# Performance work log

Hardware: AMD Instinct MI355X
Metric: run time of the kernel (lower is better)

The kernel has to match this reference:

```python
import jax, jax.numpy as jnp
import numpy as np

B, N, E = 4, 10000, 160000
NODE_DIM, EDGE_DIM, HIDDEN, HEADS = 128, 64, 256, 8
HEAD_DIM = HIDDEN // HEADS
LN_EPS = 1e-5


def setup_inputs() -> dict:
    key = jax.random.key(0)
    ks = jax.random.split(key, 11)
    s = 0.05  # stand-in for xavier scale
    return {
        "node_feat": jax.random.normal(ks[0], (B, N, NODE_DIM), dtype=jnp.float32),
        "edge_index": jax.random.randint(ks[1], (2, E), 0, N, dtype=jnp.int64),
        "edge_attr": jax.random.normal(ks[2], (B, E, EDGE_DIM), dtype=jnp.float32),
        "W_node": jax.random.normal(ks[3], (NODE_DIM, HIDDEN), dtype=jnp.float32) * s,
        "W_edge": jax.random.normal(ks[4], (EDGE_DIM, HIDDEN), dtype=jnp.float32) * s,
        "W_res": jax.random.normal(ks[5], (NODE_DIM, HIDDEN), dtype=jnp.float32) * s,
        "att_src": jax.random.normal(ks[6], (HEADS, HEAD_DIM), dtype=jnp.float32) * s,
        "att_dst": jax.random.normal(ks[7], (HEADS, HEAD_DIM), dtype=jnp.float32) * s,
        "att_edge": jax.random.normal(ks[8], (HEADS, HEAD_DIM), dtype=jnp.float32) * s,
        "ln_gamma": jnp.ones((HIDDEN,), dtype=jnp.float32),
        "ln_beta": jnp.zeros((HIDDEN,), dtype=jnp.float32),
    }


def reference(node_feat, edge_index, edge_attr, W_node, W_edge, W_res,
              att_src, att_dst, att_edge, ln_gamma, ln_beta):
    b, n, _ = node_feat.shape
    e_cnt = edge_attr.shape[1]
    src = edge_index[0]
    dst = edge_index[1]

    h = (node_feat @ W_node).reshape(b, n, HEADS, HEAD_DIM)          # [B,N,H,D]
    e = (edge_attr @ W_edge).reshape(b, e_cnt, HEADS, HEAD_DIM)       # [B,E,H,D]
    h_src = h[:, src]                                                 # [B,E,H,D]
    h_dst = h[:, dst]                                                 # [B,E,H,D]

    logits = (jnp.einsum('behd,hd->beh', h_src, att_src)
              + jnp.einsum('behd,hd->beh', h_dst, att_dst)
              + jnp.einsum('behd,hd->beh', e, att_edge))              # [B,E,H]
    logits = jax.nn.leaky_relu(logits, negative_slope=0.2)

    # segment softmax over edges grouped by dst node (edge-leading layout)
    lt = logits.transpose(1, 0, 2)                                    # [E,B,H]
    seg_max = jax.ops.segment_max(lt, dst, num_segments=n)            # [N,B,H]
    ex = jnp.exp(lt - seg_max[dst])
    seg_sum = jax.ops.segment_sum(ex, dst, num_segments=n)            # [N,B,H]
    alpha = ex / seg_sum[dst]                                         # [E,B,H]

    msg = alpha[..., None] * (h_src + e).transpose(1, 0, 2, 3)        # [E,B,H,D]
    agg = jax.ops.segment_sum(msg, dst, num_segments=n)               # [N,B,H,D]
    out = agg.transpose(1, 0, 2, 3).reshape(b, n, HIDDEN)             # [B,N,HIDDEN]

    x = out + node_feat @ W_res
    mu = jnp.mean(x, axis=-1, keepdims=True)
    var = jnp.mean(jnp.square(x - mu), axis=-1, keepdims=True)
    x = (x - mu) * jax.lax.rsqrt(var + LN_EPS) * ln_gamma + ln_beta
    return jax.nn.elu(x)
```

## Files before the change

### kernel.cpp

```cpp
#include <hip/hip_runtime.h>

#define BB 4
#define NN 10000
#define EE 160000
#define HID 256
#define NHEAD 8

typedef __attribute__((ext_vector_type(8))) short short8v;
typedef __attribute__((ext_vector_type(4))) float f32x4;

__device__ __forceinline__ unsigned short f2bf(float f) {
  unsigned u = __float_as_uint(f);
  unsigned r = (u + 0x7fffu + ((u >> 16) & 1u)) >> 16;
  return (unsigned short)r;
}
__device__ __forceinline__ float bf2f(unsigned short u) {
  return __uint_as_float(((unsigned)u) << 16);
}

__global__ __launch_bounds__(512) void k_prep(
    const float* __restrict__ We, const float* __restrict__ ae,
    const float* __restrict__ Wn, const float* __restrict__ Wr,
    float* __restrict__ What, unsigned short* __restrict__ We16,
    unsigned short* __restrict__ Bpack) {
  const int t = threadIdx.x;
  if (blockIdx.x == 32) {
    int k = t >> 3, hh = t & 7;
    float s = 0.f;
#pragma unroll
    for (int d = 0; d < 32; ++d) s += We[k * HID + hh * 32 + d] * ae[hh * 32 + d];
    What[k * NHEAD + hh] = s;
    for (int j = t; j < 64 * HID; j += 512) We16[j] = f2bf(We[j]);
    return;
  }
  if (t >= 256) return;
  const int nt = blockIdx.x;
  const int ks = t >> 6;
  const int l = t & 63;
  const int k0 = ks * 32 + (l >> 4) * 8;
  const float* __restrict__ src = (nt < 16) ? Wn : Wr;
  const int c2 = (nt * 16 + (l & 15)) & 255;
  short8v v;
#pragma unroll
  for (int e = 0; e < 8; ++e) v[e] = f2bf(src[(k0 + e) * HID + c2]);
  *reinterpret_cast<short8v*>(Bpack + ((size_t)(nt * 4 + ks) * 64 + l) * 8) = v;
}

__global__ __launch_bounds__(512) void k_projm(
    const float* __restrict__ nf, const unsigned short* __restrict__ Bpack,
    const float* __restrict__ as_, const float* __restrict__ ad_,
    unsigned short* __restrict__ h16, float* __restrict__ out,
    float* __restrict__ ssrc, float* __restrict__ sdst) {
  const int t = threadIdx.x;
  const int w = t >> 6, l = t & 63;
  const int base = blockIdx.x * 64 + (w & 3) * 16;
  const int nhalf = w >> 2;
  const int arow = base + (l & 15);
  short8v a[4];
#pragma unroll
  for (int ks = 0; ks < 4; ++ks) {
    const float* p = nf + (size_t)arow * 128 + ks * 32 + (l >> 4) * 8;
    const float4 f0 = *reinterpret_cast<const float4*>(p);
    const float4 f1 = *reinterpret_cast<const float4*>(p + 4);
    short8v v;
    v[0] = f2bf(f0.x); v[1] = f2bf(f0.y); v[2] = f2bf(f0.z); v[3] = f2bf(f0.w);
    v[4] = f2bf(f1.x); v[5] = f2bf(f1.y); v[6] = f2bf(f1.z); v[7] = f2bf(f1.w);
    a[ks] = v;
  }
  f32x4 acc[16];
#pragma unroll
  for (int i = 0; i < 16; ++i) acc[i] = (f32x4){0.f, 0.f, 0.f, 0.f};
  const short8v* bp =
      reinterpret_cast<const short8v*>(Bpack) + (size_t)nhalf * 4096 + l;
#pragma unroll
  for (int nt = 0; nt < 16; ++nt) {
#pragma unroll
    for (int ks = 0; ks < 4; ++ks) {
      const short8v bf = bp[(nt * 4 + ks) * 64];
      acc[nt] = __builtin_amdgcn_mfma_f32_16x16x32_bf16(a[ks], bf, acc[nt], 0, 0, 0);
    }
  }
  unsigned short* __restrict__ resOv = reinterpret_cast<unsigned short*>(out);
#pragma unroll
  for (int b = 0; b < 4; ++b) {
    const int bn = base + (l >> 4) * 4 + b;
    if (nhalf == 0) {
      const int bb = bn / NN, n = bn - bb * NN;
      unsigned short* __restrict__ rowp = h16 + (((size_t)n * 4 + bb) << 8);
#pragma unroll
      for (int nt = 0; nt < 16; ++nt) rowp[nt * 16 + (l & 15)] = f2bf(acc[nt][b]);
    } else {
      unsigned short* __restrict__ rowp = resOv + ((size_t)bn << 9);
#pragma unroll
      for (int nt = 0; nt < 16; ++nt) rowp[nt * 16 + (l & 15)] = f2bf(acc[nt][b]);
    }
  }
  if (nhalf == 0) {
    const int lo = l & 15;
#pragma unroll
    for (int h = 0; h < 8; ++h) {
      const float a0 = as_[h * 32 + lo], a1 = as_[h * 32 + 16 + lo];
      const float d0 = ad_[h * 32 + lo], d1 = ad_[h * 32 + 16 + lo];
#pragma unroll
      for (int rb = 0; rb < 4; ++rb) {
        float ps = acc[2 * h][rb] * a0 + acc[2 * h + 1][rb] * a1;
        float pd = acc[2 * h][rb] * d0 + acc[2 * h + 1][rb] * d1;
#pragma unroll
        for (int off = 1; off <= 8; off <<= 1) {
          ps += __shfl_xor(ps, off);
          pd += __shfl_xor(pd, off);
        }
        if (lo == 0) {
          const int bn = base + (l >> 4) * 4 + rb;
          ssrc[(size_t)bn * NHEAD + h] = ps;
          sdst[(size_t)bn * NHEAD + h] = pd;
        }
      }
    }
  }
}

__global__ void k_hist(const int* __restrict__ ei, int* __restrict__ cnt) {
  int e = blockIdx.x * 256 + threadIdx.x;
  if (e < EE) atomicAdd(&cnt[ei[EE + e]], 1);
}

__global__ __launch_bounds__(1024) void k_scan(const int* __restrict__ cnt,
                                               int* __restrict__ off) {
  __shared__ int ls[1024];
  const int t = threadIdx.x;
  int own = 0;
  int deg[10];
  if (t < 1000) {
#pragma unroll
    for (int i = 0; i < 10; ++i) { deg[i] = cnt[t * 10 + i]; own += deg[i]; }
  }
  ls[t] = own;
  __syncthreads();
  for (int s = 1; s < 1024; s <<= 1) {
    int v = 0;
    if (t >= s) v = ls[t - s];
    __syncthreads();
    if (t >= s) ls[t] += v;
    __syncthreads();
  }
  if (t < 1000) {
    int start = ls[t] - own;
#pragma unroll
    for (int i = 0; i < 10; ++i) { off[t * 10 + i] = start; start += deg[i]; }
  }
  if (t == 0) off[NN] = EE;
}

__global__ void k_scatter(const int* __restrict__ ei, const int* __restrict__ off,
                          int* __restrict__ cur, int2* __restrict__ eidx,
                          int* __restrict__ inv) {
  int e = blockIdx.x * 256 + threadIdx.x;
  if (e >= EE) return;
  int s = ei[e], d = ei[EE + e];
  int pos = off[d] + atomicAdd(&cur[d], 1);
  eidx[pos] = make_int2(e, s);
  inv[e] = pos;
}

__global__ __launch_bounds__(256) void k_elogit(
    const float* __restrict__ ea, const int* __restrict__ ei,
    const float* __restrict__ What, const float* __restrict__ ssrc,
    const float* __restrict__ sdst, const int* __restrict__ inv,
    float* __restrict__ exP) {
  __shared__ float sea[32 * 65];
  __shared__ float sw[64 * NHEAD];
  const int t = threadIdx.x;
  sw[t] = What[t];
  sw[t + 256] = What[t + 256];
  const int g0 = blockIdx.x * 32;
  const float* base = ea + (size_t)g0 * 64;
#pragma unroll
  for (int j = 0; j < 8; ++j) {
    int f = t + j * 256;
    sea[(f >> 6) * 65 + (f & 63)] = base[f];
  }
  __syncthreads();
  const int il = t >> 3, hh = t & 7;
  const int g = g0 + il;
  float acc = 0.f;
#pragma unroll
  for (int k = 0; k < 64; ++k) acc += sea[il * 65 + k] * sw[k * NHEAD + hh];
  const int b = g / EE, e = g - b * EE;
  const int src = ei[e], dst = ei[EE + e];
  float lg = ssrc[((size_t)b * NN + src) * NHEAD + hh] +
             sdst[((size_t)b * NN + dst) * NHEAD + hh] + acc;
  lg = lg > 0.f ? lg : 0.2f * lg;
  const int pos = inv[e];
  exP[(((size_t)pos * 4 + b) << 3) + hh] = __expf(lg);
}

__global__ __launch_bounds__(256) void k_agg(
    const float* __restrict__ ea, const unsigned short* __restrict__ h16,
    const float* __restrict__ exP, const int* __restrict__ off,
    const int2* __restrict__ eidx, const unsigned short* __restrict__ We16,
    const float* __restrict__ gam, const float* __restrict__ bet,
    float* __restrict__ out) {
  __shared__ float zsh[4][8 * 65];
  const int wid = threadIdx.x >> 6, l = threadIdx.x & 63;
  const int b = wid, node = blockIdx.x;
  const int start = off[node], end = off[node + 1];
  const int hq = l >> 3;
  const int hr = l & 7;
  float4 u4 = {0.f, 0.f, 0.f, 0.f};
  float z0 = 0.f, z1 = 0.f, z2 = 0.f, z3 = 0.f;
  float z4 = 0.f, z5 = 0.f, z6 = 0.f, z7 = 0.f;
  float ss = 0.f;
  const float* __restrict__ exb = exP + ((size_t)b << 3);
  const float* __restrict__ eab = ea + (size_t)b * EE * 64;
  const unsigned short* __restrict__ hb = h16 + ((size_t)b << 8);
#pragma unroll 8
  for (int i = start; i < end; ++i) {
    const int2 es = eidx[i];
    const float* exi = exb + ((size_t)i << 5);
    const float4 xa = *reinterpret_cast<const float4*>(exi);
    const float4 xb = *reinterpret_cast<const float4*>(exi + 4);
    const float exu = exi[hq];
    ss += exi[hr];
    const float eal = eab[(size_t)es.x * 64 + l];
    const ushort4 h4 =
        *reinterpret_cast<const ushort4*>(hb + ((size_t)es.y << 10) + 4 * l);
    z0 += xa.x * eal; z1 += xa.y * eal; z2 += xa.z * eal; z3 += xa.w * eal;
    z4 += xb.x * eal; z5 += xb.y * eal; z6 += xb.z * eal; z7 += xb.w * eal;
    u4.x += exu * bf2f(h4.x); u4.y += exu * bf2f(h4.y);
    u4.z += exu * bf2f(h4.z); u4.w += exu * bf2f(h4.w);
  }
  zsh[wid][0 * 65 + l] = z0; zsh[wid][1 * 65 + l] = z1;
  zsh[wid][2 * 65 + l] = z2; zsh[wid][3 * 65 + l] = z3;
  zsh[wid][4 * 65 + l] = z4; zsh[wid][5 * 65 + l] = z5;
  zsh[wid][6 * 65 + l] = z6; zsh[wid][7 * 65 + l] = z7;
  const size_t bn = (size_t)b * NN + node;
  const ushort4 r16 = *reinterpret_cast<const ushort4*>(
      reinterpret_cast<const unsigned short*>(out) + (bn << 9) + 4 * l);
#pragma unroll 8
  for (int k = 0; k < 64; ++k) {
    const float zk = zsh[wid][hq * 65 + k];
    const ushort4 wv = *reinterpret_cast<const ushort4*>(We16 + (k << 8) + 4 * l);
    u4.x += zk * bf2f(wv.x); u4.y += zk * bf2f(wv.y);
    u4.z += zk * bf2f(wv.z); u4.w += zk * bf2f(wv.w);
  }
  const float ssq = __shfl(ss, hq);
  const float sc = ssq > 0.f ? 1.f / ssq : 0.f;
  u4.x = u4.x * sc + bf2f(r16.x); u4.y = u4.y * sc + bf2f(r16.y);
  u4.z = u4.z * sc + bf2f(r16.z); u4.w = u4.w * sc + bf2f(r16.w);
  float s1 = u4.x + u4.y + u4.z + u4.w;
  float s2 = u4.x * u4.x + u4.y * u4.y + u4.z * u4.z + u4.w * u4.w;
#pragma unroll
  for (int off2 = 1; off2 <= 32; off2 <<= 1) {
    s1 += __shfl_xor(s1, off2);
    s2 += __shfl_xor(s2, off2);
  }
  const float mu = s1 * (1.f / HID);
  const float var = s2 * (1.f / HID) - mu * mu;
  const float rstd = rsqrtf(var + 1e-5f);
  const float4 g4 = reinterpret_cast<const float4*>(gam)[l];
  const float4 b4 = reinterpret_cast<const float4*>(bet)[l];
  float4 y;
  y.x = (u4.x - mu) * rstd * g4.x + b4.x;
  y.y = (u4.y - mu) * rstd * g4.y + b4.y;
  y.z = (u4.z - mu) * rstd * g4.z + b4.z;
  y.w = (u4.w - mu) * rstd * g4.w + b4.w;
  y.x = y.x > 0.f ? y.x : expm1f(y.x);
  y.y = y.y > 0.f ? y.y : expm1f(y.y);
  y.z = y.z > 0.f ? y.z : expm1f(y.z);
  y.w = y.w > 0.f ? y.w : expm1f(y.w);
  *reinterpret_cast<float4*>(out + (bn << 8) + 4 * l) = y;
}

extern "C" void kernel_launch(void* const* d_in, const int* in_sizes, int n_in,
                              void* d_out, int out_size, void* d_ws, size_t ws_size,
                              hipStream_t stream) {
  const float* nf   = (const float*)d_in[0];
  const int*   ei   = (const int*)d_in[1];
  const float* eatt = (const float*)d_in[2];
  const float* Wn   = (const float*)d_in[3];
  const float* We   = (const float*)d_in[4];
  const float* Wr   = (const float*)d_in[5];
  const float* as_  = (const float*)d_in[6];
  const float* ad_  = (const float*)d_in[7];
  const float* ae_  = (const float*)d_in[8];
  const float* gam  = (const float*)d_in[9];
  const float* bet  = (const float*)d_in[10];
  float* out = (float*)d_out;

  char* ws = (char*)d_ws;
  size_t o = 0;
  auto alloc = [&](size_t bytes) -> void* {
    void* p = ws + o;
    o += (bytes + 255) & ~(size_t)255;
    return p;
  };
  unsigned short* h16  = (unsigned short*)alloc((size_t)BB * NN * HID * 2);
  float* ssrc   = (float*)alloc((size_t)BB * NN * NHEAD * 4);
  float* sdst   = (float*)alloc((size_t)BB * NN * NHEAD * 4);
  float* What   = (float*)alloc(64 * NHEAD * 4);
  unsigned short* We16 = (unsigned short*)alloc(64 * HID * 2);
  float* exP    = (float*)alloc((size_t)BB * EE * NHEAD * 4);
  size_t cnt_off = o;
  int*  cnt     = (int*)alloc(NN * 4);
  int*  cur     = (int*)alloc(NN * 4);
  size_t cnt_bytes = o - cnt_off;
  int*  offn    = (int*)alloc((NN + 1) * 4);
  int2* eidx    = (int2*)alloc((size_t)EE * 8);
  int*  inv     = (int*)alloc((size_t)EE * 4);
  unsigned short* Bpack = (unsigned short*)alloc((size_t)512 * 128 * 2);

  hipLaunchKernelGGL(k_prep, dim3(33), dim3(512), 0, stream,
                     We, ae_, Wn, Wr, What, We16, Bpack);
  hipLaunchKernelGGL(k_projm, dim3(BB * NN / 64), dim3(512), 0, stream,
                     nf, Bpack, as_, ad_, h16, out, ssrc, sdst);
  hipMemsetAsync(ws + cnt_off, 0, cnt_bytes, stream);
  hipLaunchKernelGGL(k_hist, dim3((EE + 255) / 256), dim3(256), 0, stream, ei, cnt);
  hipLaunchKernelGGL(k_scan, dim3(1), dim3(1024), 0, stream, cnt, offn);
  hipLaunchKernelGGL(k_scatter, dim3((EE + 255) / 256), dim3(256), 0, stream,
                     ei, offn, cur, eidx, inv);
  hipLaunchKernelGGL(k_elogit, dim3(BB * EE / 32), dim3(256), 0, stream,
                     eatt, ei, What, ssrc, sdst, inv, exP);
  hipLaunchKernelGGL(k_agg, dim3(NN), dim3(256), 0, stream,
                     eatt, h16, exP, offn, eidx, We16, gam, bet, out);
}
```

Before: 282.9 us.

## Fold memset and histogram into prep/projection kernels; aggregate two nodes per block

The memset of the count and cursor arrays moves into extra blocks of the prep kernel, and the degree histogram moves into extra blocks of the projection kernel. This removes one memset and one kernel launch. The aggregation kernel now handles two destination nodes per block and interleaves their edge loops, so more independent gathers are in flight and each We16 load is reused for both nodes. The cost is higher register pressure and fewer blocks in the aggregation kernel.

```diff
diff --git a/kernel.cpp b/kernel.cpp
--- a/kernel.cpp
+++ b/kernel.cpp
@@ -22,8 +22,16 @@
     const float* __restrict__ We, const float* __restrict__ ae,
     const float* __restrict__ Wn, const float* __restrict__ Wr,
     float* __restrict__ What, unsigned short* __restrict__ We16,
-    unsigned short* __restrict__ Bpack) {
+    unsigned short* __restrict__ Bpack, int* __restrict__ cnt,
+    int* __restrict__ cur) {
   const int t = threadIdx.x;
+  if (blockIdx.x >= 33) {
+    const int zb = blockIdx.x - 33;
+    int* __restrict__ dst = (zb < 20) ? cnt : cur;
+    const int idx = (zb % 20) * 512 + t;
+    if (idx < NN) dst[idx] = 0;
+    return;
+  }
   if (blockIdx.x == 32) {
     int k = t >> 3, hh = t & 7;
     float s = 0.f;
@@ -50,8 +58,14 @@
     const float* __restrict__ nf, const unsigned short* __restrict__ Bpack,
     const float* __restrict__ as_, const float* __restrict__ ad_,
     unsigned short* __restrict__ h16, float* __restrict__ out,
-    float* __restrict__ ssrc, float* __restrict__ sdst) {
+    float* __restrict__ ssrc, float* __restrict__ sdst,
+    const int* __restrict__ ei, int* __restrict__ cnt) {
   const int t = threadIdx.x;
+  if (blockIdx.x >= 625) {
+    const int e = (blockIdx.x - 625) * 512 + t;
+    if (e < EE) atomicAdd(&cnt[ei[EE + e]], 1);
+    return;
+  }
   const int w = t >> 6, l = t & 63;
   const int base = blockIdx.x * 64 + (w & 3) * 16;
   const int nhalf = w >> 2;
@@ -118,11 +132,6 @@
       }
     }
   }
-}
-
-__global__ void k_hist(const int* __restrict__ ei, int* __restrict__ cnt) {
-  int e = blockIdx.x * 256 + threadIdx.x;
-  if (e < EE) atomicAdd(&cnt[ei[EE + e]], 1);
 }
 
 __global__ __launch_bounds__(1024) void k_scan(const int* __restrict__ cnt,
@@ -195,81 +204,125 @@
   exP[(((size_t)pos * 4 + b) << 3) + hh] = __expf(lg);
 }
 
+#define AGG_BODY(i, u4, z0, z1, z2, z3, z4, z5, z6, z7, ss)                    \
+  {                                                                            \
+    const int2 es = eidx[i];                                                   \
+    const float* exi = exb + ((size_t)(i) << 5);                               \
+    const float4 xa = *reinterpret_cast<const float4*>(exi);                   \
+    const float4 xb = *reinterpret_cast<const float4*>(exi + 4);               \
+    const float exu = exi[hq];                                                 \
+    ss += exi[hr];                                                             \
+    const float eal = eab[(size_t)es.x * 64 + l];                              \
+    const ushort4 h4 =                                                         \
+        *reinterpret_cast<const ushort4*>(hb + ((size_t)es.y << 10) + 4 * l);  \
+    z0 += xa.x * eal; z1 += xa.y * eal; z2 += xa.z * eal; z3 += xa.w * eal;    \
+    z4 += xb.x * eal; z5 += xb.y * eal; z6 += xb.z * eal; z7 += xb.w * eal;    \
+    u4.x += exu * bf2f(h4.x); u4.y += exu * bf2f(h4.y);                        \
+    u4.z += exu * bf2f(h4.z); u4.w += exu * bf2f(h4.w);                        \
+  }
+
 __global__ __launch_bounds__(256) void k_agg(
     const float* __restrict__ ea, const unsigned short* __restrict__ h16,
     const float* __restrict__ exP, const int* __restrict__ off,
     const int2* __restrict__ eidx, const unsigned short* __restrict__ We16,
     const float* __restrict__ gam, const float* __restrict__ bet,
     float* __restrict__ out) {
-  __shared__ float zsh[4][8 * 65];
+  __shared__ float zshA[4][8 * 65];
+  __shared__ float zshB[4][8 * 65];
   const int wid = threadIdx.x >> 6, l = threadIdx.x & 63;
-  const int b = wid, node = blockIdx.x;
-  const int start = off[node], end = off[node + 1];
+  const int b = wid;
+  const int nodeA = blockIdx.x * 2, nodeB = nodeA + 1;
+  const int sA = off[nodeA], eAe = off[nodeA + 1], eBe = off[nodeB + 1];
+  const int sB = eAe;
   const int hq = l >> 3;
   const int hr = l & 7;
-  float4 u4 = {0.f, 0.f, 0.f, 0.f};
-  float z0 = 0.f, z1 = 0.f, z2 = 0.f, z3 = 0.f;
-  float z4 = 0.f, z5 = 0.f, z6 = 0.f, z7 = 0.f;
-  float ss = 0.f;
+  float4 uA = {0.f, 0.f, 0.f, 0.f}, uB = {0.f, 0.f, 0.f, 0.f};
+  float zA0 = 0.f, zA1 = 0.f, zA2 = 0.f, zA3 = 0.f;
+  float zA4 = 0.f, zA5 = 0.f, zA6 = 0.f, zA7 = 0.f;
+  float zB0 = 0.f, zB1 = 0.f, zB2 = 0.f, zB3 = 0.f;
+  float zB4 = 0.f, zB5 = 0.f, zB6 = 0.f, zB7 = 0.f;
+  float ssA = 0.f, ssB = 0.f;
   const float* __restrict__ exb = exP + ((size_t)b << 3);
   const float* __restrict__ eab = ea + (size_t)b * EE * 64;
   const unsigned short* __restrict__ hb = h16 + ((size_t)b << 8);
-#pragma unroll 8
-  for (int i = start; i < end; ++i) {
-    const int2 es = eidx[i];
-    const float* exi = exb + ((size_t)i << 5);
-    const float4 xa = *reinterpret_cast<const float4*>(exi);
-    const float4 xb = *reinterpret_cast<const float4*>(exi + 4);
-    const float exu = exi[hq];
-    ss += exi[hr];
-    const float eal = eab[(size_t)es.x * 64 + l];
-    const ushort4 h4 =
-        *reinterpret_cast<const ushort4*>(hb + ((size_t)es.y << 10) + 4 * l);
-    z0 += xa.x * eal; z1 += xa.y * eal; z2 += xa.z * eal; z3 += xa.w * eal;
-    z4 += xb.x * eal; z5 += xb.y * eal; z6 += xb.z * eal; z7 += xb.w * eal;
-    u4.x += exu * bf2f(h4.x); u4.y += exu * bf2f(h4.y);
-    u4.z += exu * bf2f(h4.z); u4.w += exu * bf2f(h4.w);
-  }
-  zsh[wid][0 * 65 + l] = z0; zsh[wid][1 * 65 + l] = z1;
-  zsh[wid][2 * 65 + l] = z2; zsh[wid][3 * 65 + l] = z3;
-  zsh[wid][4 * 65 + l] = z4; zsh[wid][5 * 65 + l] = z5;
-  zsh[wid][6 * 65 + l] = z6; zsh[wid][7 * 65 + l] = z7;
-  const size_t bn = (size_t)b * NN + node;
-  const ushort4 r16 = *reinterpret_cast<const ushort4*>(
-      reinterpret_cast<const unsigned short*>(out) + (bn << 9) + 4 * l);
+  const int nA = eAe - sA, nB = eBe - sB;
+  const int nmin = nA < nB ? nA : nB;
+  for (int j = 0; j < nmin; ++j) {
+    AGG_BODY(sA + j, uA, zA0, zA1, zA2, zA3, zA4, zA5, zA6, zA7, ssA);
+    AGG_BODY(sB + j, uB, zB0, zB1, zB2, zB3, zB4, zB5, zB6, zB7, ssB);
+  }
+  for (int j = nmin; j < nA; ++j)
+    AGG_BODY(sA + j, uA, zA0, zA1, zA2, zA3, zA4, zA5, zA6, zA7, ssA);
+  for (int j = nmin; j < nB; ++j)
+    AGG_BODY(sB + j, uB, zB0, zB1, zB2, zB3, zB4, zB5, zB6, zB7, ssB);
+  zshA[wid][0 * 65 + l] = zA0; zshA[wid][1 * 65 + l] = zA1;
+  zshA[wid][2 * 65 + l] = zA2; zshA[wid][3 * 65 + l] = zA3;
+  zshA[wid][4 * 65 + l] = zA4; zshA[wid][5 * 65 + l] = zA5;
+  zshA[wid][6 * 65 + l] = zA6; zshA[wid][7 * 65 + l] = zA7;
+  zshB[wid][0 * 65 + l] = zB0; zshB[wid][1 * 65 + l] = zB1;
+  zshB[wid][2 * 65 + l] = zB2; zshB[wid][3 * 65 + l] = zB3;
+  zshB[wid][4 * 65 + l] = zB4; zshB[wid][5 * 65 + l] = zB5;
+  zshB[wid][6 * 65 + l] = zB6; zshB[wid][7 * 65 + l] = zB7;
+  const size_t bnA = (size_t)b * NN + nodeA;
+  const size_t bnB = bnA + 1;
+  const unsigned short* __restrict__ ov =
+      reinterpret_cast<const unsigned short*>(out);
+  const ushort4 rA = *reinterpret_cast<const ushort4*>(ov + (bnA << 9) + 4 * l);
+  const ushort4 rB = *reinterpret_cast<const ushort4*>(ov + (bnB << 9) + 4 * l);
 #pragma unroll 8
   for (int k = 0; k < 64; ++k) {
-    const float zk = zsh[wid][hq * 65 + k];
+    const float zkA = zshA[wid][hq * 65 + k];
+    const float zkB = zshB[wid][hq * 65 + k];
     const ushort4 wv = *reinterpret_cast<const ushort4*>(We16 + (k << 8) + 4 * l);
-    u4.x += zk * bf2f(wv.x); u4.y += zk * bf2f(wv.y);
-    u4.z += zk * bf2f(wv.z); u4.w += zk * bf2f(wv.w);
-  }
-  const float ssq = __shfl(ss, hq);
-  const float sc = ssq > 0.f ? 1.f / ssq : 0.f;
-  u4.x = u4.x * sc + bf2f(r16.x); u4.y = u4.y * sc + bf2f(r16.y);
-  u4.z = u4.z * sc + bf2f(r16.z); u4.w = u4.w * sc + bf2f(r16.w);
-  float s1 = u4.x + u4.y + u4.z + u4.w;
-  float s2 = u4.x * u4.x + u4.y * u4.y + u4.z * u4.z + u4.w * u4.w;
+    const float w0 = bf2f(wv.x), w1 = bf2f(wv.y), w2 = bf2f(wv.z), w3 = bf2f(wv.w);
+    uA.x += zkA * w0; uA.y += zkA * w1; uA.z += zkA * w2; uA.w += zkA * w3;
+    uB.x += zkB * w0; uB.y += zkB * w1; uB.z += zkB * w2; uB.w += zkB * w3;
+  }
+  const float sqA = __shfl(ssA, hq), sqB = __shfl(ssB, hq);
+  const float scA = sqA > 0.f ? 1.f / sqA : 0.f;
+  const float scB = sqB > 0.f ? 1.f / sqB : 0.f;
+  uA.x = uA.x * scA + bf2f(rA.x); uA.y = uA.y * scA + bf2f(rA.y);
+  uA.z = uA.z * scA + bf2f(rA.z); uA.w = uA.w * scA + bf2f(rA.w);
+  uB.x = uB.x * scB + bf2f(rB.x); uB.y = uB.y * scB + bf2f(rB.y);
+  uB.z = uB.z * scB + bf2f(rB.z); uB.w = uB.w * scB + bf2f(rB.w);
+  float s1A = uA.x + uA.y + uA.z + uA.w;
+  float s2A = uA.x * uA.x + uA.y * uA.y + uA.z * uA.z + uA.w * uA.w;
+  float s1B = uB.x + uB.y + uB.z + uB.w;
+  float s2B = uB.x * uB.x + uB.y * uB.y + uB.z * uB.z + uB.w * uB.w;
 #pragma unroll
   for (int off2 = 1; off2 <= 32; off2 <<= 1) {
-    s1 += __shfl_xor(s1, off2);
-    s2 += __shfl_xor(s2, off2);
-  }
-  const float mu = s1 * (1.f / HID);
-  const float var = s2 * (1.f / HID) - mu * mu;
-  const float rstd = rsqrtf(var + 1e-5f);
+    s1A += __shfl_xor(s1A, off2);
+    s2A += __shfl_xor(s2A, off2);
+    s1B += __shfl_xor(s1B, off2);
+    s2B += __shfl_xor(s2B, off2);
+  }
+  const float muA = s1A * (1.f / HID);
+  const float varA = s2A * (1.f / HID) - muA * muA;
+  const float rsA = rsqrtf(varA + 1e-5f);
+  const float muB = s1B * (1.f / HID);
+  const float varB = s2B * (1.f / HID) - muB * muB;
+  const float rsB = rsqrtf(varB + 1e-5f);
   const float4 g4 = reinterpret_cast<const float4*>(gam)[l];
   const float4 b4 = reinterpret_cast<const float4*>(bet)[l];
-  float4 y;
-  y.x = (u4.x - mu) * rstd * g4.x + b4.x;
-  y.y = (u4.y - mu) * rstd * g4.y + b4.y;
-  y.z = (u4.z - mu) * rstd * g4.z + b4.z;
-  y.w = (u4.w - mu) * rstd * g4.w + b4.w;
-  y.x = y.x > 0.f ? y.x : expm1f(y.x);
-  y.y = y.y > 0.f ? y.y : expm1f(y.y);
-  y.z = y.z > 0.f ? y.z : expm1f(y.z);
-  y.w = y.w > 0.f ? y.w : expm1f(y.w);
-  *reinterpret_cast<float4*>(out + (bn << 8) + 4 * l) = y;
+  float4 yA, yB;
+  yA.x = (uA.x - muA) * rsA * g4.x + b4.x;
+  yA.y = (uA.y - muA) * rsA * g4.y + b4.y;
+  yA.z = (uA.z - muA) * rsA * g4.z + b4.z;
+  yA.w = (uA.w - muA) * rsA * g4.w + b4.w;
+  yB.x = (uB.x - muB) * rsB * g4.x + b4.x;
+  yB.y = (uB.y - muB) * rsB * g4.y + b4.y;
+  yB.z = (uB.z - muB) * rsB * g4.z + b4.z;
+  yB.w = (uB.w - muB) * rsB * g4.w + b4.w;
+  yA.x = yA.x > 0.f ? yA.x : expm1f(yA.x);
+  yA.y = yA.y > 0.f ? yA.y : expm1f(yA.y);
+  yA.z = yA.z > 0.f ? yA.z : expm1f(yA.z);
+  yA.w = yA.w > 0.f ? yA.w : expm1f(yA.w);
+  yB.x = yB.x > 0.f ? yB.x : expm1f(yB.x);
+  yB.y = yB.y > 0.f ? yB.y : expm1f(yB.y);
+  yB.z = yB.z > 0.f ? yB.z : expm1f(yB.z);
+  yB.w = yB.w > 0.f ? yB.w : expm1f(yB.w);
+  *reinterpret_cast<float4*>(out + (bnA << 8) + 4 * l) = yA;
+  *reinterpret_cast<float4*>(out + (bnB << 8) + 4 * l) = yB;
 }
 
 extern "C" void kernel_launch(void* const* d_in, const int* in_sizes, int n_in,
@@ -301,26 +354,22 @@
   float* What   = (float*)alloc(64 * NHEAD * 4);
   unsigned short* We16 = (unsigned short*)alloc(64 * HID * 2);
   float* exP    = (float*)alloc((size_t)BB * EE * NHEAD * 4);
-  size_t cnt_off = o;
   int*  cnt     = (int*)alloc(NN * 4);
   int*  cur     = (int*)alloc(NN * 4);
-  size_t cnt_bytes = o - cnt_off;
   int*  offn    = (int*)alloc((NN + 1) * 4);
   int2* eidx    = (int2*)alloc((size_t)EE * 8);
   int*  inv     = (int*)alloc((size_t)EE * 4);
   unsigned short* Bpack = (unsigned short*)alloc((size_t)512 * 128 * 2);
 
-  hipLaunchKernelGGL(k_prep, dim3(33), dim3(512), 0, stream,
-                     We, ae_, Wn, Wr, What, We16, Bpack);
-  hipLaunchKernelGGL(k_projm, dim3(BB * NN / 64), dim3(512), 0, stream,
-                     nf, Bpack, as_, ad_, h16, out, ssrc, sdst);
-  hipMemsetAsync(ws + cnt_off, 0, cnt_bytes, stream);
-  hipLaunchKernelGGL(k_hist, dim3((EE + 255) / 256), dim3(256), 0, stream, ei, cnt);
+  hipLaunchKernelGGL(k_prep, dim3(73), dim3(512), 0, stream,
+                     We, ae_, Wn, Wr, What, We16, Bpack, cnt, cur);
+  hipLaunchKernelGGL(k_projm, dim3(625 + (EE + 511) / 512), dim3(512), 0, stream,
+                     nf, Bpack, as_, ad_, h16, out, ssrc, sdst, ei, cnt);
   hipLaunchKernelGGL(k_scan, dim3(1), dim3(1024), 0, stream, cnt, offn);
   hipLaunchKernelGGL(k_scatter, dim3((EE + 255) / 256), dim3(256), 0, stream,
                      ei, offn, cur, eidx, inv);
   hipLaunchKernelGGL(k_elogit, dim3(BB * EE / 32), dim3(256), 0, stream,
                      eatt, ei, What, ssrc, sdst, inv, exP);
-  hipLaunchKernelGGL(k_agg, dim3(NN), dim3(256), 0, stream,
+  hipLaunchKernelGGL(k_agg, dim3(NN / 2), dim3(256), 0, stream,
                      eatt, h16, exP, offn, eidx, We16, gam, bet, out);
 }
```

Measured after the change: 242.2 us, median of 2. 14.4% less time.

## Fuse counter zeroing and histogram into existing kernels; process four nodes per agg block

Applied to the files above, without the earlier changes.

Zeroing of the degree counters moves into extra blocks of the prep kernel, and the destination histogram moves into extra blocks of the projection kernel. This removes a memset and a separate kernel launch. The aggregation kernel now handles four destination nodes per block, interleaving their edge loops so more independent gathers are in flight, with the gamma/beta loads shared across nodes. The cost is much higher register pressure from four sets of accumulators, and divergence when the four nodes have different degrees.

```diff
diff --git a/kernel.cpp b/kernel.cpp
--- a/kernel.cpp
+++ b/kernel.cpp
@@ -22,8 +22,16 @@
     const float* __restrict__ We, const float* __restrict__ ae,
     const float* __restrict__ Wn, const float* __restrict__ Wr,
     float* __restrict__ What, unsigned short* __restrict__ We16,
-    unsigned short* __restrict__ Bpack) {
+    unsigned short* __restrict__ Bpack, int* __restrict__ cnt,
+    int* __restrict__ cur) {
   const int t = threadIdx.x;
+  if (blockIdx.x >= 33) {
+    const int zb = blockIdx.x - 33;
+    int* __restrict__ dst = (zb < 20) ? cnt : cur;
+    const int idx = (zb % 20) * 512 + t;
+    if (idx < NN) dst[idx] = 0;
+    return;
+  }
   if (blockIdx.x == 32) {
     int k = t >> 3, hh = t & 7;
     float s = 0.f;
@@ -50,8 +58,14 @@
     const float* __restrict__ nf, const unsigned short* __restrict__ Bpack,
     const float* __restrict__ as_, const float* __restrict__ ad_,
     unsigned short* __restrict__ h16, float* __restrict__ out,
-    float* __restrict__ ssrc, float* __restrict__ sdst) {
+    float* __restrict__ ssrc, float* __restrict__ sdst,
+    const int* __restrict__ ei, int* __restrict__ cnt) {
   const int t = threadIdx.x;
+  if (blockIdx.x >= 625) {
+    const int e = (blockIdx.x - 625) * 512 + t;
+    if (e < EE) atomicAdd(&cnt[ei[EE + e]], 1);
+    return;
+  }
   const int w = t >> 6, l = t & 63;
   const int base = blockIdx.x * 64 + (w & 3) * 16;
   const int nhalf = w >> 2;
@@ -118,11 +132,6 @@
       }
     }
   }
-}
-
-__global__ void k_hist(const int* __restrict__ ei, int* __restrict__ cnt) {
-  int e = blockIdx.x * 256 + threadIdx.x;
-  if (e < EE) atomicAdd(&cnt[ei[EE + e]], 1);
 }
 
 __global__ __launch_bounds__(1024) void k_scan(const int* __restrict__ cnt,
@@ -195,51 +204,37 @@
   exP[(((size_t)pos * 4 + b) << 3) + hh] = __expf(lg);
 }
 
-__global__ __launch_bounds__(256) void k_agg(
-    const float* __restrict__ ea, const unsigned short* __restrict__ h16,
-    const float* __restrict__ exP, const int* __restrict__ off,
-    const int2* __restrict__ eidx, const unsigned short* __restrict__ We16,
-    const float* __restrict__ gam, const float* __restrict__ bet,
-    float* __restrict__ out) {
-  __shared__ float zsh[4][8 * 65];
-  const int wid = threadIdx.x >> 6, l = threadIdx.x & 63;
-  const int b = wid, node = blockIdx.x;
-  const int start = off[node], end = off[node + 1];
-  const int hq = l >> 3;
-  const int hr = l & 7;
-  float4 u4 = {0.f, 0.f, 0.f, 0.f};
-  float z0 = 0.f, z1 = 0.f, z2 = 0.f, z3 = 0.f;
-  float z4 = 0.f, z5 = 0.f, z6 = 0.f, z7 = 0.f;
-  float ss = 0.f;
-  const float* __restrict__ exb = exP + ((size_t)b << 3);
-  const float* __restrict__ eab = ea + (size_t)b * EE * 64;
-  const unsigned short* __restrict__ hb = h16 + ((size_t)b << 8);
-#pragma unroll 8
-  for (int i = start; i < end; ++i) {
-    const int2 es = eidx[i];
-    const float* exi = exb + ((size_t)i << 5);
-    const float4 xa = *reinterpret_cast<const float4*>(exi);
-    const float4 xb = *reinterpret_cast<const float4*>(exi + 4);
-    const float exu = exi[hq];
-    ss += exi[hr];
-    const float eal = eab[(size_t)es.x * 64 + l];
-    const ushort4 h4 =
-        *reinterpret_cast<const ushort4*>(hb + ((size_t)es.y << 10) + 4 * l);
-    z0 += xa.x * eal; z1 += xa.y * eal; z2 += xa.z * eal; z3 += xa.w * eal;
-    z4 += xb.x * eal; z5 += xb.y * eal; z6 += xb.z * eal; z7 += xb.w * eal;
-    u4.x += exu * bf2f(h4.x); u4.y += exu * bf2f(h4.y);
-    u4.z += exu * bf2f(h4.z); u4.w += exu * bf2f(h4.w);
-  }
-  zsh[wid][0 * 65 + l] = z0; zsh[wid][1 * 65 + l] = z1;
-  zsh[wid][2 * 65 + l] = z2; zsh[wid][3 * 65 + l] = z3;
-  zsh[wid][4 * 65 + l] = z4; zsh[wid][5 * 65 + l] = z5;
-  zsh[wid][6 * 65 + l] = z6; zsh[wid][7 * 65 + l] = z7;
-  const size_t bn = (size_t)b * NN + node;
+#define AGG_BODY(i, u4, z0, z1, z2, z3, z4, z5, z6, z7, ss)                    \
+  {                                                                            \
+    const int2 es = eidx[i];                                                   \
+    const float* exi = exb + ((size_t)(i) << 5);                               \
+    const float4 xa = *reinterpret_cast<const float4*>(exi);                   \
+    const float4 xb = *reinterpret_cast<const float4*>(exi + 4);               \
+    const float exu = exi[hq];                                                 \
+    ss += exi[hr];                                                             \
+    const float eal = eab[(size_t)es.x * 64 + l];                              \
+    const ushort4 h4 =                                                         \
+        *reinterpret_cast<const ushort4*>(hb + ((size_t)es.y << 10) + 4 * l);  \
+    z0 += xa.x * eal; z1 += xa.y * eal; z2 += xa.z * eal; z3 += xa.w * eal;    \
+    z4 += xb.x * eal; z5 += xb.y * eal; z6 += xb.z * eal; z7 += xb.w * eal;    \
+    u4.x += exu * bf2f(h4.x); u4.y += exu * bf2f(h4.y);                        \
+    u4.z += exu * bf2f(h4.z); u4.w += exu * bf2f(h4.w);                        \
+  }
+
+__device__ __forceinline__ void agg_epilogue(
+    float* __restrict__ zrow, int l, int hq, float4 u4, float ss,
+    float z0, float z1, float z2, float z3, float z4, float z5, float z6,
+    float z7, size_t bn, const unsigned short* __restrict__ We16,
+    float4 g4, float4 b4, float* __restrict__ out) {
+  zrow[0 * 65 + l] = z0; zrow[1 * 65 + l] = z1;
+  zrow[2 * 65 + l] = z2; zrow[3 * 65 + l] = z3;
+  zrow[4 * 65 + l] = z4; zrow[5 * 65 + l] = z5;
+  zrow[6 * 65 + l] = z6; zrow[7 * 65 + l] = z7;
   const ushort4 r16 = *reinterpret_cast<const ushort4*>(
       reinterpret_cast<const unsigned short*>(out) + (bn << 9) + 4 * l);
 #pragma unroll 8
   for (int k = 0; k < 64; ++k) {
-    const float zk = zsh[wid][hq * 65 + k];
+    const float zk = zrow[hq * 65 + k];
     const ushort4 wv = *reinterpret_cast<const ushort4*>(We16 + (k << 8) + 4 * l);
     u4.x += zk * bf2f(wv.x); u4.y += zk * bf2f(wv.y);
     u4.z += zk * bf2f(wv.z); u4.w += zk * bf2f(wv.w);
@@ -258,8 +253,6 @@
   const float mu = s1 * (1.f / HID);
   const float var = s2 * (1.f / HID) - mu * mu;
   const float rstd = rsqrtf(var + 1e-5f);
-  const float4 g4 = reinterpret_cast<const float4*>(gam)[l];
-  const float4 b4 = reinterpret_cast<const float4*>(bet)[l];
   float4 y;
   y.x = (u4.x - mu) * rstd * g4.x + b4.x;
   y.y = (u4.y - mu) * rstd * g4.y + b4.y;
@@ -270,6 +263,58 @@
   y.z = y.z > 0.f ? y.z : expm1f(y.z);
   y.w = y.w > 0.f ? y.w : expm1f(y.w);
   *reinterpret_cast<float4*>(out + (bn << 8) + 4 * l) = y;
+}
+
+__global__ __launch_bounds__(256) void k_agg(
+    const float* __restrict__ ea, const unsigned short* __restrict__ h16,
+    const float* __restrict__ exP, const int* __restrict__ off,
+    const int2* __restrict__ eidx, const unsigned short* __restrict__ We16,
+    const float* __restrict__ gam, const float* __restrict__ bet,
+    float* __restrict__ out) {
+  __shared__ float zsh[4][8 * 65];
+  const int wid = threadIdx.x >> 6, l = threadIdx.x & 63;
+  const int b = wid;
+  const int node0 = blockIdx.x * 4;
+  const int s0 = off[node0], s1 = off[node0 + 1], s2 = off[node0 + 2],
+            s3 = off[node0 + 3], s4 = off[node0 + 4];
+  const int n0 = s1 - s0, n1 = s2 - s1, n2 = s3 - s2, n3 = s4 - s3;
+  int nmax = n0 > n1 ? n0 : n1;
+  nmax = nmax > n2 ? nmax : n2;
+  nmax = nmax > n3 ? nmax : n3;
+  const int hq = l >> 3;
+  const int hr = l & 7;
+  float4 uA = {0.f, 0.f, 0.f, 0.f}, uB = {0.f, 0.f, 0.f, 0.f};
+  float4 uC = {0.f, 0.f, 0.f, 0.f}, uD = {0.f, 0.f, 0.f, 0.f};
+  float zA0 = 0.f, zA1 = 0.f, zA2 = 0.f, zA3 = 0.f;
+  float zA4 = 0.f, zA5 = 0.f, zA6 = 0.f, zA7 = 0.f;
+  float zB0 = 0.f, zB1 = 0.f, zB2 = 0.f, zB3 = 0.f;
+  float zB4 = 0.f, zB5 = 0.f, zB6 = 0.f, zB7 = 0.f;
+  float zC0 = 0.f, zC1 = 0.f, zC2 = 0.f, zC3 = 0.f;
+  float zC4 = 0.f, zC5 = 0.f, zC6 = 0.f, zC7 = 0.f;
+  float zD0 = 0.f, zD1 = 0.f, zD2 = 0.f, zD3 = 0.f;
+  float zD4 = 0.f, zD5 = 0.f, zD6 = 0.f, zD7 = 0.f;
+  float ssA = 0.f, ssB = 0.f, ssC = 0.f, ssD = 0.f;
+  const float* __restrict__ exb = exP + ((size_t)b << 3);
+  const float* __restrict__ eab = ea + (size_t)b * EE * 64;
+  const unsigned short* __restrict__ hb = h16 + ((size_t)b << 8);
+  for (int j = 0; j < nmax; ++j) {
+    if (j < n0) AGG_BODY(s0 + j, uA, zA0, zA1, zA2, zA3, zA4, zA5, zA6, zA7, ssA);
+    if (j < n1) AGG_BODY(s1 + j, uB, zB0, zB1, zB2, zB3, zB4, zB5, zB6, zB7, ssB);
+    if (j < n2) AGG_BODY(s2 + j, uC, zC0, zC1, zC2, zC3, zC4, zC5, zC6, zC7, ssC);
+    if (j < n3) AGG_BODY(s3 + j, uD, zD0, zD1, zD2, zD3, zD4, zD5, zD6, zD7, ssD);
+  }
+  const float4 g4 = reinterpret_cast<const float4*>(gam)[l];
+  const float4 b4 = reinterpret_cast<const float4*>(bet)[l];
+  float* __restrict__ zrow = zsh[wid];
+  const size_t bn0 = (size_t)b * NN + node0;
+  agg_epilogue(zrow, l, hq, uA, ssA, zA0, zA1, zA2, zA3, zA4, zA5, zA6, zA7,
+               bn0 + 0, We16, g4, b4, out);
+  agg_epilogue(zrow, l, hq, uB, ssB, zB0, zB1, zB2, zB3, zB4, zB5, zB6, zB7,
+               bn0 + 1, We16, g4, b4, out);
+  agg_epilogue(zrow, l, hq, uC, ssC, zC0, zC1, zC2, zC3, zC4, zC5, zC6, zC7,
+               bn0 + 2, We16, g4, b4, out);
+  agg_epilogue(zrow, l, hq, uD, ssD, zD0, zD1, zD2, zD3, zD4, zD5, zD6, zD7,
+               bn0 + 3, We16, g4, b4, out);
 }
 
 extern "C" void kernel_launch(void* const* d_in, const int* in_sizes, int n_in,
@@ -301,26 +346,22 @@
   float* What   = (float*)alloc(64 * NHEAD * 4);
   unsigned short* We16 = (unsigned short*)alloc(64 * HID * 2);
   float* exP    = (float*)alloc((size_t)BB * EE * NHEAD * 4);
-  size_t cnt_off = o;
   int*  cnt     = (int*)alloc(NN * 4);
   int*  cur     = (int*)alloc(NN * 4);
-  size_t cnt_bytes = o - cnt_off;
   int*  offn    = (int*)alloc((NN + 1) * 4);
   int2* eidx    = (int2*)alloc((size_t)EE * 8);
   int*  inv     = (int*)alloc((size_t)EE * 4);
   unsigned short* Bpack = (unsigned short*)alloc((size_t)512 * 128 * 2);
 
-  hipLaunchKernelGGL(k_prep, dim3(33), dim3(512), 0, stream,
-                     We, ae_, Wn, Wr, What, We16, Bpack);
-  hipLaunchKernelGGL(k_projm, dim3(BB * NN / 64), dim3(512), 0, stream,
-                     nf, Bpack, as_, ad_, h16, out, ssrc, sdst);
-  hipMemsetAsync(ws + cnt_off, 0, cnt_bytes, stream);
-  hipLaunchKernelGGL(k_hist, dim3((EE + 255) / 256), dim3(256), 0, stream, ei, cnt);
+  hipLaunchKernelGGL(k_prep, dim3(73), dim3(512), 0, stream,
+                     We, ae_, Wn, Wr, What, We16, Bpack, cnt, cur);
+  hipLaunchKernelGGL(k_projm, dim3(625 + (EE + 511) / 512), dim3(512), 0, stream,
+                     nf, Bpack, as_, ad_, h16, out, ssrc, sdst, ei, cnt);
   hipLaunchKernelGGL(k_scan, dim3(1), dim3(1024), 0, stream, cnt, offn);
   hipLaunchKernelGGL(k_scatter, dim3((EE + 255) / 256), dim3(256), 0, stream,
                      ei, offn, cur, eidx, inv);
   hipLaunchKernelGGL(k_elogit, dim3(BB * EE / 32), dim3(256), 0, stream,
                      eatt, ei, What, ssrc, sdst, inv, exP);
-  hipLaunchKernelGGL(k_agg, dim3(NN), dim3(256), 0, stream,
+  hipLaunchKernelGGL(k_agg, dim3(NN / 4), dim3(256), 0, stream,
                      eatt, h16, exP, offn, eidx, We16, gam, bet, out);
 }
```

New measurement: 336.6 us. +19.0%, slower.

## Fold memset and histogram into existing kernels, batch agg loads by four

Applied to the files above, without the earlier changes.

Zeroing of the count and cursor arrays moves into extra blocks of k_prep, and the destination histogram moves into extra blocks of k_projm. This removes a memset and a separate kernel launch. The aggregation loop is restructured to issue the loads for four edges before doing their arithmetic, which exposes more memory-level parallelism, and it gains a launch_bounds occupancy hint. The cost is higher register pressure in k_agg, plus an edge-index buffer enlarged by four entries.

```diff
diff --git a/kernel.cpp b/kernel.cpp
--- a/kernel.cpp
+++ b/kernel.cpp
@@ -22,8 +22,16 @@
     const float* __restrict__ We, const float* __restrict__ ae,
     const float* __restrict__ Wn, const float* __restrict__ Wr,
     float* __restrict__ What, unsigned short* __restrict__ We16,
-    unsigned short* __restrict__ Bpack) {
+    unsigned short* __restrict__ Bpack, int* __restrict__ cnt,
+    int* __restrict__ cur) {
   const int t = threadIdx.x;
+  if (blockIdx.x >= 33) {
+    const int zb = blockIdx.x - 33;
+    int* __restrict__ dst = (zb < 20) ? cnt : cur;
+    const int idx = (zb % 20) * 512 + t;
+    if (idx < NN) dst[idx] = 0;
+    return;
+  }
   if (blockIdx.x == 32) {
     int k = t >> 3, hh = t & 7;
     float s = 0.f;
@@ -50,8 +58,14 @@
     const float* __restrict__ nf, const unsigned short* __restrict__ Bpack,
     const float* __restrict__ as_, const float* __restrict__ ad_,
     unsigned short* __restrict__ h16, float* __restrict__ out,
-    float* __restrict__ ssrc, float* __restrict__ sdst) {
+    float* __restrict__ ssrc, float* __restrict__ sdst,
+    const int* __restrict__ ei, int* __restrict__ cnt) {
   const int t = threadIdx.x;
+  if (blockIdx.x >= 625) {
+    const int e = (blockIdx.x - 625) * 512 + t;
+    if (e < EE) atomicAdd(&cnt[ei[EE + e]], 1);
+    return;
+  }
   const int w = t >> 6, l = t & 63;
   const int base = blockIdx.x * 64 + (w & 3) * 16;
   const int nhalf = w >> 2;
@@ -118,11 +132,6 @@
       }
     }
   }
-}
-
-__global__ void k_hist(const int* __restrict__ ei, int* __restrict__ cnt) {
-  int e = blockIdx.x * 256 + threadIdx.x;
-  if (e < EE) atomicAdd(&cnt[ei[EE + e]], 1);
 }
 
 __global__ __launch_bounds__(1024) void k_scan(const int* __restrict__ cnt,
@@ -195,7 +204,35 @@
   exP[(((size_t)pos * 4 + b) << 3) + hh] = __expf(lg);
 }
 
-__global__ __launch_bounds__(256) void k_agg(
+struct EData {
+  float4 xa, xb;
+  float exu, ssv, eal;
+  ushort4 h4;
+};
+
+#define LOADD(i, es, d)                                                        \
+  {                                                                            \
+    const float* exi = exb + ((size_t)(i) << 5);                               \
+    d.xa = *reinterpret_cast<const float4*>(exi);                              \
+    d.xb = *reinterpret_cast<const float4*>(exi + 4);                          \
+    d.exu = exi[hq];                                                           \
+    d.ssv = exi[hr];                                                           \
+    d.eal = eab[(size_t)(es).x * 64 + l];                                      \
+    d.h4 = *reinterpret_cast<const ushort4*>(hb + ((size_t)(es).y << 10) + 4 * l); \
+  }
+
+#define COMP(d)                                                                \
+  {                                                                            \
+    z0 += d.xa.x * d.eal; z1 += d.xa.y * d.eal;                                \
+    z2 += d.xa.z * d.eal; z3 += d.xa.w * d.eal;                                \
+    z4 += d.xb.x * d.eal; z5 += d.xb.y * d.eal;                                \
+    z6 += d.xb.z * d.eal; z7 += d.xb.w * d.eal;                                \
+    ss += d.ssv;                                                               \
+    u4.x += d.exu * bf2f(d.h4.x); u4.y += d.exu * bf2f(d.h4.y);                \
+    u4.z += d.exu * bf2f(d.h4.z); u4.w += d.exu * bf2f(d.h4.w);                \
+  }
+
+__global__ __launch_bounds__(256, 4) void k_agg(
     const float* __restrict__ ea, const unsigned short* __restrict__ h16,
     const float* __restrict__ exP, const int* __restrict__ off,
     const int2* __restrict__ eidx, const unsigned short* __restrict__ We16,
@@ -214,21 +251,26 @@
   const float* __restrict__ exb = exP + ((size_t)b << 3);
   const float* __restrict__ eab = ea + (size_t)b * EE * 64;
   const unsigned short* __restrict__ hb = h16 + ((size_t)b << 8);
-#pragma unroll 8
-  for (int i = start; i < end; ++i) {
-    const int2 es = eidx[i];
-    const float* exi = exb + ((size_t)i << 5);
-    const float4 xa = *reinterpret_cast<const float4*>(exi);
-    const float4 xb = *reinterpret_cast<const float4*>(exi + 4);
-    const float exu = exi[hq];
-    ss += exi[hr];
-    const float eal = eab[(size_t)es.x * 64 + l];
-    const ushort4 h4 =
-        *reinterpret_cast<const ushort4*>(hb + ((size_t)es.y << 10) + 4 * l);
-    z0 += xa.x * eal; z1 += xa.y * eal; z2 += xa.z * eal; z3 += xa.w * eal;
-    z4 += xb.x * eal; z5 += xb.y * eal; z6 += xb.z * eal; z7 += xb.w * eal;
-    u4.x += exu * bf2f(h4.x); u4.y += exu * bf2f(h4.y);
-    u4.z += exu * bf2f(h4.z); u4.w += exu * bf2f(h4.w);
+  int j = start;
+  const int n4 = start + ((end - start) & ~3);
+  for (; j < n4; j += 4) {
+    const int2 e0 = eidx[j], e1 = eidx[j + 1];
+    const int2 e2 = eidx[j + 2], e3 = eidx[j + 3];
+    EData d0, d1, d2, d3;
+    LOADD(j, e0, d0);
+    LOADD(j + 1, e1, d1);
+    LOADD(j + 2, e2, d2);
+    LOADD(j + 3, e3, d3);
+    COMP(d0);
+    COMP(d1);
+    COMP(d2);
+    COMP(d3);
+  }
+  for (; j < end; ++j) {
+    const int2 es = eidx[j];
+    EData d;
+    LOADD(j, es, d);
+    COMP(d);
   }
   zsh[wid][0 * 65 + l] = z0; zsh[wid][1 * 65 + l] = z1;
   zsh[wid][2 * 65 + l] = z2; zsh[wid][3 * 65 + l] = z3;
@@ -301,21 +343,17 @@
   float* What   = (float*)alloc(64 * NHEAD * 4);
   unsigned short* We16 = (unsigned short*)alloc(64 * HID * 2);
   float* exP    = (float*)alloc((size_t)BB * EE * NHEAD * 4);
-  size_t cnt_off = o;
   int*  cnt     = (int*)alloc(NN * 4);
   int*  cur     = (int*)alloc(NN * 4);
-  size_t cnt_bytes = o - cnt_off;
   int*  offn    = (int*)alloc((NN + 1) * 4);
-  int2* eidx    = (int2*)alloc((size_t)EE * 8);
+  int2* eidx    = (int2*)alloc((size_t)(EE + 4) * 8);
   int*  inv     = (int*)alloc((size_t)EE * 4);
   unsigned short* Bpack = (unsigned short*)alloc((size_t)512 * 128 * 2);
 
-  hipLaunchKernelGGL(k_prep, dim3(33), dim3(512), 0, stream,
-                     We, ae_, Wn, Wr, What, We16, Bpack);
-  hipLaunchKernelGGL(k_projm, dim3(BB * NN / 64), dim3(512), 0, stream,
-                     nf, Bpack, as_, ad_, h16, out, ssrc, sdst);
-  hipMemsetAsync(ws + cnt_off, 0, cnt_bytes, stream);
-  hipLaunchKernelGGL(k_hist, dim3((EE + 255) / 256), dim3(256), 0, stream, ei, cnt);
+  hipLaunchKernelGGL(k_prep, dim3(73), dim3(512), 0, stream,
+                     We, ae_, Wn, Wr, What, We16, Bpack, cnt, cur);
+  hipLaunchKernelGGL(k_projm, dim3(625 + (EE + 511) / 512), dim3(512), 0, stream,
+                     nf, Bpack, as_, ad_, h16, out, ssrc, sdst, ei, cnt);
   hipLaunchKernelGGL(k_scan, dim3(1), dim3(1024), 0, stream, cnt, offn);
   hipLaunchKernelGGL(k_scatter, dim3((EE + 255) / 256), dim3(256), 0, stream,
                      ei, offn, cur, eidx, inv);
```

Measured after the change: 275.1 us. -2.8%, faster.
